# Kernel optimization log

Hardware: AMD Instinct MI355X
Metric: run time of the kernel (lower is better)

Reference implementation:

```python
import jax, jax.numpy as jnp
import numpy as np


def setup_inputs() -> dict:
    key = jax.random.key(0)
    k0, k1, k2, k3 = jax.random.split(key, 4)
    B, S, D, F, E = 2, 2048, 1024, 4096, 8
    scale = 0.02
    return {
        "x": jax.random.normal(k0, (B, S, D), jnp.float32),
        "gate_w": jax.random.normal(k1, (E, D), jnp.float32) * scale,
        "gate_b": jnp.zeros((E,), jnp.float32),
        "w1": jax.random.normal(k2, (E, D, F), jnp.float32) * scale,
        "b1": jnp.zeros((E, F), jnp.float32),
        "w2": jax.random.normal(k3, (E, F, D), jnp.float32) * scale,
        "b2": jnp.zeros((E, D), jnp.float32),
        "top_k": 2,
    }


def reference(x, gate_w, gate_b, w1, b1, w2, b2, top_k):
    B, S, D = x.shape
    E = gate_w.shape[0]
    xt = x.reshape(-1, D)                                   # [T, D]
    T = xt.shape[0]

    # Router: softmax over gate logits, then top-k and renormalize.
    gate_probs = jax.nn.softmax(xt @ gate_w.T + gate_b, axis=-1)   # [T, E]
    weights, selected = jax.lax.top_k(gate_probs, top_k)           # [T, k]
    weights = weights / jnp.sum(weights, axis=-1, keepdims=True)

    # Per-token combine weights over experts (zero where not selected),
    # equivalent to the per-expert gather/scatter loop in the original.
    combine = jnp.zeros((T, E), x.dtype).at[
        jnp.arange(T)[:, None], selected
    ].add(weights)                                                 # [T, E]

    # Expert MLPs (dense over experts, masked combine).
    h = jax.nn.silu(jnp.einsum("td,edf->etf", xt, w1) + b1[:, None, :])  # [E, T, F]
    expert_out = jnp.einsum("etf,efd->etd", h, w2) + b2[:, None, :]      # [E, T, D]
    out = jnp.einsum("etd,te->td", expert_out, combine)                  # [T, D]
    return out.reshape(B, S, D)
```

## Files before the change

kernel.cpp:

```cpp
#include <hip/hip_runtime.h>

#define T_TOK 4096
#define DIM   1024
#define FDIM  4096
#define NEXP  8

typedef __bf16 bf16x8 __attribute__((ext_vector_type(8)));
typedef __bf16 bf16x4 __attribute__((ext_vector_type(4)));
typedef float  f32x4  __attribute__((ext_vector_type(4)));

__device__ __forceinline__ void glds16(const void* g, void* l) {
    __builtin_amdgcn_global_load_lds(
        (const __attribute__((address_space(1))) void*)g,
        (__attribute__((address_space(3))) void*)l, 16, 0, 0);
}

__device__ __forceinline__ int xcd_swz(int phys, int total) {
    int q = total >> 3, r = total & 7;
    int x = phys & 7, i = phys >> 3;
    return (x < r ? x * (q + 1) : r * (q + 1) + (x - r) * q) + i;
}

__global__ __launch_bounds__(64)
void moe_router(const float* __restrict__ x,
                const float* __restrict__ gw,
                const float* __restrict__ gb,
                const int*   __restrict__ topk_p,
                int*   __restrict__ counts,
                int*   __restrict__ bucket,
                float* __restrict__ bweight,
                __bf16* __restrict__ xb) {
    const int t = blockIdx.x;
    const int lane = threadIdx.x;
    float part[NEXP];
#pragma unroll
    for (int e = 0; e < NEXP; ++e) part[e] = 0.f;
    const float* xrow = x + (size_t)t * DIM;
    __bf16* xbrow = xb + (size_t)t * DIM;
#pragma unroll
    for (int r = 0; r < 4; ++r) {
        int c = r * 256 + lane * 4;
        float4 v = *(const float4*)&xrow[c];
        bf16x4 o; o[0]=(__bf16)v.x; o[1]=(__bf16)v.y; o[2]=(__bf16)v.z; o[3]=(__bf16)v.w;
        *(bf16x4*)&xbrow[c] = o;
#pragma unroll
        for (int e = 0; e < NEXP; ++e) {
            float4 g = *(const float4*)&gw[e * DIM + c];
            part[e] += v.x*g.x + v.y*g.y + v.z*g.z + v.w*g.w;
        }
    }
#pragma unroll
    for (int off = 32; off > 0; off >>= 1) {
#pragma unroll
        for (int e = 0; e < NEXP; ++e) part[e] += __shfl_xor(part[e], off);
    }
    if (lane == 0) {
        int k = topk_p[0];
        if (k < 1) k = 1;
        if (k > NEXP) k = NEXP;
        float p[NEXP];
        float mx = -1e30f;
#pragma unroll
        for (int e = 0; e < NEXP; ++e) {
            p[e] = part[e] + gb[e];
            mx = fmaxf(mx, p[e]);
        }
#pragma unroll
        for (int e = 0; e < NEXP; ++e) p[e] = __expf(p[e] - mx);
        bool used[NEXP];
#pragma unroll
        for (int e = 0; e < NEXP; ++e) used[e] = false;
        int sel[NEXP]; float selp[NEXP]; float wsum = 0.f;
        for (int j = 0; j < k; ++j) {
            int best = 0; float bv = -1.f;
            for (int e = 0; e < NEXP; ++e)
                if (!used[e] && p[e] > bv) { bv = p[e]; best = e; }
            used[best] = true; sel[j] = best; selp[j] = bv; wsum += bv;
        }
        for (int j = 0; j < k; ++j) {
            int e = sel[j];
            int pos = atomicAdd(&counts[e], 1);
            bucket[e * T_TOK + pos]  = t;
            bweight[e * T_TOK + pos] = selp[j] / wsum;
        }
    }
}

__global__ __launch_bounds__(256)
void transpose_cvt(const float* __restrict__ in, __bf16* __restrict__ out,
                   int R, int C) {
    const size_t zo = (size_t)blockIdx.z * R * C;
    in += zo; out += zo;
    __shared__ float ts[64][65];
    const int c0 = blockIdx.x * 64, r0 = blockIdx.y * 64;
    const int t = threadIdx.x;
    const int rr = t >> 2, cc4 = (t & 3) * 16;
    const float* src = in + (size_t)(r0 + rr) * C + c0 + cc4;
#pragma unroll
    for (int i = 0; i < 4; ++i) {
        float4 v = *(const float4*)(src + i * 4);
        ts[rr][cc4 + i*4 + 0] = v.x; ts[rr][cc4 + i*4 + 1] = v.y;
        ts[rr][cc4 + i*4 + 2] = v.z; ts[rr][cc4 + i*4 + 3] = v.w;
    }
    __syncthreads();
    const int oc = rr, orc = cc4;
    bf16x8 o0, o1;
#pragma unroll
    for (int i = 0; i < 8; ++i) o0[i] = (__bf16)ts[orc + i][oc];
#pragma unroll
    for (int i = 0; i < 8; ++i) o1[i] = (__bf16)ts[orc + 8 + i][oc];
    __bf16* dst = out + (size_t)(c0 + oc) * R + r0 + orc;
    *(bf16x8*)dst = o0;
    *(bf16x8*)(dst + 8) = o1;
}

__global__ __launch_bounds__(64)
void build_work(const int* __restrict__ counts, int* __restrict__ hdr) {
    __shared__ int off1[NEXP + 1];
    const int lane = threadIdx.x;
    if (lane == 0) {
        int a = 0;
        for (int e = 0; e < NEXP; ++e) {
            off1[e] = a;
            a += (counts[e] + 255) >> 8;
        }
        off1[NEXP] = a;
        hdr[0] = a;
    }
    __syncthreads();
    for (int e = 0; e < NEXP; ++e) {
        int n1 = off1[e + 1] - off1[e];
        for (int j = lane; j < n1; j += 64) hdr[8 + off1[e] + j] = (e << 16) | j;
    }
}


__global__ __launch_bounds__(512, 2)
void moe_gemm1(const __bf16* __restrict__ xb,
               const __bf16* __restrict__ w1t,
               const float*  __restrict__ b1,
               const int*    __restrict__ counts,
               const int*    __restrict__ bucket,
               const int*    __restrict__ hdr,
               __bf16* __restrict__ H) {
    __shared__ __align__(16) char sb[3 * 32768];
    __shared__ int tok_s[256];
    const int tid = threadIdx.x;
    const int wave = tid >> 6, lane = tid & 63;
    const int wm = wave & 1, wn = wave >> 1;
    const int quad = lane >> 4, l15 = lane & 15;
    const int lrow = lane >> 2;
    const int rr  = tid >> 2;
    const int srh = ((tid & 3) ^ ((tid >> 3) & 3)) * 8;
    const int swz16 = (((lane >> 4) ^ ((lane >> 1) & 3)) << 4);
    const int aoff = (wm * 128 + l15) * 64 + swz16;
    const int boff = (wn * 64  + l15) * 64 + swz16;

    const int NT = DIM / 32;
    const int n1 = hdr[0];
    const int total = n1 * (FDIM / 256);
    for (int phys = blockIdx.x; phys < total; phys += gridDim.x) {
        const int u = xcd_swz(phys, total);
        const int entry = hdr[8 + (u % n1)];
        const int e = entry >> 16, tile = entry & 0xffff;
        const int nb = (u / n1) * 256;
        const int cnt = counts[e];
        for (int r = tid; r < 256; r += 512) {
            int rw = tile * 256 + r;
            if (rw >= cnt) rw = cnt - 1;
            tok_s[r] = bucket[e * T_TOK + rw];
        }
        __syncthreads();

        const __bf16* pa0 = xb + (size_t)tok_s[rr]       * DIM + srh;
        const __bf16* pa1 = xb + (size_t)tok_s[rr + 128] * DIM + srh;
        const __bf16* pb0 = w1t + ((size_t)e * FDIM + nb + rr) * DIM + srh;
        const __bf16* pb1 = pb0 + (size_t)128 * DIM;

        f32x4 acc[8][4];
#pragma unroll
        for (int i = 0; i < 8; ++i)
#pragma unroll
            for (int j = 0; j < 4; ++j) acc[i][j] = (f32x4){0.f,0.f,0.f,0.f};

#pragma unroll
        for (int p = 0; p < 2; ++p) {
            char* db = sb + p * 32768;
            const int ko = p * 32;
            glds16(pa0 + ko, db + wave * 1024);
            glds16(pa1 + ko, db + 8192 + wave * 1024);
            glds16(pb0 + ko, db + 16384 + wave * 1024);
            glds16(pb1 + ko, db + 24576 + wave * 1024);
        }

        int bc = 0, bn = 2;
#pragma unroll 1
        for (int t = 0; t < NT; ++t) {
            if (t + 2 < NT) {
                char* db = sb + bn * 32768;
                const int ko = (t + 2) * 32;
                glds16(pa0 + ko, db + wave * 1024);
                glds16(pa1 + ko, db + 8192 + wave * 1024);
                glds16(pb0 + ko, db + 16384 + wave * 1024);
                glds16(pb1 + ko, db + 24576 + wave * 1024);
                asm volatile("s_waitcnt vmcnt(8)" ::: "memory");
            } else if (t + 2 == NT) {
                asm volatile("s_waitcnt vmcnt(4)" ::: "memory");
            } else {
                asm volatile("s_waitcnt vmcnt(0)" ::: "memory");
            }
            __builtin_amdgcn_s_barrier();
            asm volatile("" ::: "memory");

            const char* Ab = sb + bc * 32768;
            const char* Bb = Ab + 16384;
            bf16x8 af[8], bfr[4];
#pragma unroll
            for (int i = 0; i < 8; ++i)
                af[i] = *(const bf16x8*)(Ab + aoff + i * 1024);
#pragma unroll
            for (int j = 0; j < 4; ++j)
                bfr[j] = *(const bf16x8*)(Bb + boff + j * 1024);
            __builtin_amdgcn_s_setprio(1);
#pragma unroll
            for (int i = 0; i < 8; ++i)
#pragma unroll
                for (int j = 0; j < 4; ++j)
                    acc[i][j] = __builtin_amdgcn_mfma_f32_16x16x32_bf16(
                        af[i], bfr[j], acc[i][j], 0, 0, 0);
            __builtin_amdgcn_s_setprio(0);

            asm volatile("" ::: "memory");
            __builtin_amdgcn_s_barrier();
            bc = (bc == 2) ? 0 : bc + 1;
            bn = (bn == 2) ? 0 : bn + 1;
        }

        __bf16* stg = (__bf16*)(sb + wave * 2304);
        const float* b1e = b1 + e * FDIM + nb + wn * 64;
#pragma unroll
        for (int i = 0; i < 8; ++i) {
#pragma unroll
            for (int j = 0; j < 4; ++j) {
                float bias = b1e[j * 16 + l15];
#pragma unroll
                for (int r = 0; r < 4; ++r) {
                    float v = acc[i][j][r] + bias;
                    float s = v / (1.f + __expf(-v));
                    stg[(quad*4 + r) * 72 + j*16 + l15] = (__bf16)s;
                }
            }
            int prow = tile * 256 + wm * 128 + i * 16 + lrow;
            if (prow < cnt) {
                bf16x8 v0 = *(const bf16x8*)&stg[lrow * 72 + (lane & 3) * 16];
                bf16x8 v1 = *(const bf16x8*)&stg[lrow * 72 + (lane & 3) * 16 + 8];
                __bf16* dst = H + (size_t)(e * T_TOK + prow) * FDIM
                              + nb + wn * 64 + (lane & 3) * 16;
                *(bf16x8*)dst = v0;
                *(bf16x8*)(dst + 8) = v1;
            }
        }
        __syncthreads();
    }
}

#define KSPLIT 2
#define KHALF  (FDIM / KSPLIT)

__global__ __launch_bounds__(512, 2)
void moe_gemm2(const __bf16* __restrict__ H,
               const __bf16* __restrict__ w2t,
               const float*  __restrict__ b2,
               const int*    __restrict__ counts,
               const int*    __restrict__ bucket,
               const float*  __restrict__ bweight,
               const int*    __restrict__ hdr,
               float* __restrict__ out) {
    __shared__ __align__(16) char sb[3 * 32768];
    __shared__ int   tok_s[256];
    __shared__ float w_s[256];
    const int tid = threadIdx.x;
    const int wave = tid >> 6, lane = tid & 63;
    const int wm = wave & 1, wn = wave >> 1;
    const int quad = lane >> 4, l15 = lane & 15;
    const int rr  = tid >> 2;
    const int srh = ((tid & 3) ^ ((tid >> 3) & 3)) * 8;
    const int swz16 = (((lane >> 4) ^ ((lane >> 1) & 3)) << 4);
    const int aoff = (wm * 128 + l15) * 64 + swz16;
    const int boff = (wn * 64  + l15) * 64 + swz16;

    const int NT = KHALF / 32;
    const int n1 = hdr[0];
    const int total = n1 * (DIM / 256) * KSPLIT;
    for (int phys = blockIdx.x; phys < total; phys += gridDim.x) {
        const int u = xcd_swz(phys, total);
        const int entry = hdr[8 + (u % n1)];
        const int e = entry >> 16, tile = entry & 0xffff;
        const int rest = u / n1;
        const int nb = (rest & 3) * 256;
        const int kc = rest >> 2;
        const int cnt = counts[e];
        for (int r = tid; r < 256; r += 512) {
            int rw = tile * 256 + r;
            int rc = rw < cnt ? rw : cnt - 1;
            tok_s[r] = bucket[e * T_TOK + rc];
            w_s[r]   = bweight[e * T_TOK + rc];
        }
        __syncthreads();

        const size_t kbase = (size_t)kc * KHALF;
        const __bf16* pa0 = H + (size_t)(e * T_TOK + tile * 256 + rr) * FDIM + kbase + srh;
        const __bf16* pa1 = pa0 + (size_t)128 * FDIM;
        const __bf16* pb0 = w2t + ((size_t)e * DIM + nb + rr) * FDIM + kbase + srh;
        const __bf16* pb1 = pb0 + (size_t)128 * FDIM;

        f32x4 acc[8][4];
#pragma unroll
        for (int i = 0; i < 8; ++i)
#pragma unroll
            for (int j = 0; j < 4; ++j) acc[i][j] = (f32x4){0.f,0.f,0.f,0.f};

#pragma unroll
        for (int p = 0; p < 2; ++p) {
            char* db = sb + p * 32768;
            const int ko = p * 32;
            glds16(pa0 + ko, db + wave * 1024);
            glds16(pa1 + ko, db + 8192 + wave * 1024);
            glds16(pb0 + ko, db + 16384 + wave * 1024);
            glds16(pb1 + ko, db + 24576 + wave * 1024);
        }

        int bc = 0, bn = 2;
#pragma unroll 1
        for (int t = 0; t < NT; ++t) {
            if (t + 2 < NT) {
                char* db = sb + bn * 32768;
                const int ko = (t + 2) * 32;
                glds16(pa0 + ko, db + wave * 1024);
                glds16(pa1 + ko, db + 8192 + wave * 1024);
                glds16(pb0 + ko, db + 16384 + wave * 1024);
                glds16(pb1 + ko, db + 24576 + wave * 1024);
                asm volatile("s_waitcnt vmcnt(8)" ::: "memory");
            } else if (t + 2 == NT) {
                asm volatile("s_waitcnt vmcnt(4)" ::: "memory");
            } else {
                asm volatile("s_waitcnt vmcnt(0)" ::: "memory");
            }
            __builtin_amdgcn_s_barrier();
            asm volatile("" ::: "memory");

            const char* Ab = sb + bc * 32768;
            const char* Bb = Ab + 16384;
            bf16x8 af[8], bfr[4];
#pragma unroll
            for (int i = 0; i < 8; ++i)
                af[i] = *(const bf16x8*)(Ab + aoff + i * 1024);
#pragma unroll
            for (int j = 0; j < 4; ++j)
                bfr[j] = *(const bf16x8*)(Bb + boff + j * 1024);
            __builtin_amdgcn_s_setprio(1);
#pragma unroll
            for (int i = 0; i < 8; ++i)
#pragma unroll
                for (int j = 0; j < 4; ++j)
                    acc[i][j] = __builtin_amdgcn_mfma_f32_16x16x32_bf16(
                        af[i], bfr[j], acc[i][j], 0, 0, 0);
            __builtin_amdgcn_s_setprio(0);

            asm volatile("" ::: "memory");
            __builtin_amdgcn_s_barrier();
            bc = (bc == 2) ? 0 : bc + 1;
            bn = (bn == 2) ? 0 : bn + 1;
        }

        float bias[4];
#pragma unroll
        for (int j = 0; j < 4; ++j)
            bias[j] = (kc == 0) ? b2[e * DIM + nb + wn * 64 + j * 16 + l15] : 0.f;
#pragma unroll
        for (int i = 0; i < 8; ++i)
#pragma unroll
            for (int j = 0; j < 4; ++j)
#pragma unroll
                for (int r = 0; r < 4; ++r) {
                    int m = wm * 128 + i * 16 + quad * 4 + r;
                    int prow = tile * 256 + m;
                    if (prow < cnt) {
                        int dc = nb + wn * 64 + j * 16 + l15;
                        float v = acc[i][j][r] + bias[j];
                        atomicAdd(&out[(size_t)tok_s[m] * DIM + dc], w_s[m] * v);
                    }
                }
        __syncthreads();
    }
}

extern "C" void kernel_launch(void* const* d_in, const int* in_sizes, int n_in,
                              void* d_out, int out_size, void* d_ws, size_t ws_size,
                              hipStream_t stream) {
    const float* x  = (const float*)d_in[0];
    const float* gw = (const float*)d_in[1];
    const float* gb = (const float*)d_in[2];
    const float* w1 = (const float*)d_in[3];
    const float* b1 = (const float*)d_in[4];
    const float* w2 = (const float*)d_in[5];
    const float* b2 = (const float*)d_in[6];
    const int* topk = (const int*)d_in[7];
    float* out = (float*)d_out;

    char* ws = (char*)d_ws;
    size_t off = 0;
    int* counts = (int*)(ws + off);    off += 256;
    int* bucket = (int*)(ws + off);    off += (size_t)NEXP * T_TOK * 4;
    float* bw   = (float*)(ws + off);  off += (size_t)NEXP * T_TOK * 4;
    int* hdr    = (int*)(ws + off);    off += 4096;
    off = (off + 255) & ~(size_t)255;
    __bf16* xb  = (__bf16*)(ws + off); off += (size_t)T_TOK * DIM * 2;
    __bf16* w1t = (__bf16*)(ws + off); off += (size_t)NEXP * DIM * FDIM * 2;
    __bf16* w2t = (__bf16*)(ws + off); off += (size_t)NEXP * FDIM * DIM * 2;
    __bf16* H   = (__bf16*)(ws + off);

    hipMemsetAsync(counts, 0, 256, stream);
    hipMemsetAsync(out, 0, (size_t)out_size * 4, stream);

    moe_router<<<T_TOK, 64, 0, stream>>>(x, gw, gb, topk, counts, bucket, bw, xb);
    transpose_cvt<<<dim3(FDIM/64, DIM/64, NEXP), 256, 0, stream>>>(w1, w1t, DIM, FDIM);
    transpose_cvt<<<dim3(DIM/64, FDIM/64, NEXP), 256, 0, stream>>>(w2, w2t, FDIM, DIM);
    build_work<<<1, 64, 0, stream>>>(counts, hdr);

    moe_gemm1<<<256, 512, 0, stream>>>(xb, w1t, b1, counts, bucket, hdr, H);
    moe_gemm2<<<256, 512, 0, stream>>>(H, w2t, b2, counts, bucket, bw, hdr, out);
}
```

Baseline: 833.0 us.

## Deepen the LDS prefetch pipeline to four stages and hand-issue the ds_read_b128 loads

Both expert GEMM kernels grow the shared-memory ring from 3 to 4 tiles. The global-to-LDS prefetch now runs three K-steps ahead, with adjusted vmcnt waits, so more global-load latency can hide behind MFMA work. Fragment loads become inline-asm ds_read_b128 instructions with immediate offsets, followed by one lgkmcnt(0) wait and a sched_barrier, which removes per-load address arithmetic. The cost is more LDS per block (128KB) and a fixed schedule that stops the compiler from overlapping LDS reads with MFMAs.

```diff
diff --git a/kernel.cpp b/kernel.cpp
--- a/kernel.cpp
+++ b/kernel.cpp
@@ -8,12 +8,16 @@
 typedef __bf16 bf16x8 __attribute__((ext_vector_type(8)));
 typedef __bf16 bf16x4 __attribute__((ext_vector_type(4)));
 typedef float  f32x4  __attribute__((ext_vector_type(4)));
+typedef const __attribute__((address_space(3))) char* lds3;
 
 __device__ __forceinline__ void glds16(const void* g, void* l) {
     __builtin_amdgcn_global_load_lds(
         (const __attribute__((address_space(1))) void*)g,
         (__attribute__((address_space(3))) void*)l, 16, 0, 0);
 }
+
+#define DSR(dst, a, imm) \
+    asm volatile("ds_read_b128 %0, %1 offset:" #imm : "=v"(dst) : "v"(a) : "memory")
 
 __device__ __forceinline__ int xcd_swz(int phys, int total) {
     int q = total >> 3, r = total & 7;
@@ -143,7 +147,7 @@
                const int*    __restrict__ bucket,
                const int*    __restrict__ hdr,
                __bf16* __restrict__ H) {
-    __shared__ __align__(16) char sb[3 * 32768];
+    __shared__ __align__(16) char sb[4 * 32768];
     __shared__ int tok_s[256];
     const int tid = threadIdx.x;
     const int wave = tid >> 6, lane = tid & 63;
@@ -154,7 +158,8 @@
     const int srh = ((tid & 3) ^ ((tid >> 3) & 3)) * 8;
     const int swz16 = (((lane >> 4) ^ ((lane >> 1) & 3)) << 4);
     const int aoff = (wm * 128 + l15) * 64 + swz16;
-    const int boff = (wn * 64  + l15) * 64 + swz16;
+    const int boff = 16384 + (wn * 64 + l15) * 64 + swz16;
+    lds3 s3 = (lds3)sb;
 
     const int NT = DIM / 32;
     const int n1 = hdr[0];
@@ -184,7 +189,7 @@
             for (int j = 0; j < 4; ++j) acc[i][j] = (f32x4){0.f,0.f,0.f,0.f};
 
 #pragma unroll
-        for (int p = 0; p < 2; ++p) {
+        for (int p = 0; p < 3; ++p) {
             char* db = sb + p * 32768;
             const int ko = p * 32;
             glds16(pa0 + ko, db + wave * 1024);
@@ -193,16 +198,18 @@
             glds16(pb1 + ko, db + 24576 + wave * 1024);
         }
 
-        int bc = 0, bn = 2;
 #pragma unroll 1
         for (int t = 0; t < NT; ++t) {
-            if (t + 2 < NT) {
-                char* db = sb + bn * 32768;
-                const int ko = (t + 2) * 32;
+            const int bc = t & 3;
+            if (t + 3 < NT) {
+                char* db = sb + ((t + 3) & 3) * 32768;
+                const int ko = (t + 3) * 32;
                 glds16(pa0 + ko, db + wave * 1024);
                 glds16(pa1 + ko, db + 8192 + wave * 1024);
                 glds16(pb0 + ko, db + 16384 + wave * 1024);
                 glds16(pb1 + ko, db + 24576 + wave * 1024);
+                asm volatile("s_waitcnt vmcnt(12)" ::: "memory");
+            } else if (t + 3 == NT) {
                 asm volatile("s_waitcnt vmcnt(8)" ::: "memory");
             } else if (t + 2 == NT) {
                 asm volatile("s_waitcnt vmcnt(4)" ::: "memory");
@@ -210,17 +217,19 @@
                 asm volatile("s_waitcnt vmcnt(0)" ::: "memory");
             }
             __builtin_amdgcn_s_barrier();
-            asm volatile("" ::: "memory");
-
-            const char* Ab = sb + bc * 32768;
-            const char* Bb = Ab + 16384;
+
+            lds3 a3 = s3 + bc * 32768 + aoff;
+            lds3 b3 = s3 + bc * 32768 + boff;
             bf16x8 af[8], bfr[4];
-#pragma unroll
-            for (int i = 0; i < 8; ++i)
-                af[i] = *(const bf16x8*)(Ab + aoff + i * 1024);
-#pragma unroll
-            for (int j = 0; j < 4; ++j)
-                bfr[j] = *(const bf16x8*)(Bb + boff + j * 1024);
+            DSR(af[0], a3, 0);    DSR(af[1], a3, 1024);
+            DSR(af[2], a3, 2048); DSR(af[3], a3, 3072);
+            DSR(af[4], a3, 4096); DSR(af[5], a3, 5120);
+            DSR(af[6], a3, 6144); DSR(af[7], a3, 7168);
+            DSR(bfr[0], b3, 0);    DSR(bfr[1], b3, 1024);
+            DSR(bfr[2], b3, 2048); DSR(bfr[3], b3, 3072);
+            asm volatile("s_waitcnt lgkmcnt(0)" ::: "memory");
+            __builtin_amdgcn_sched_barrier(0);
+
             __builtin_amdgcn_s_setprio(1);
 #pragma unroll
             for (int i = 0; i < 8; ++i)
@@ -229,11 +238,7 @@
                     acc[i][j] = __builtin_amdgcn_mfma_f32_16x16x32_bf16(
                         af[i], bfr[j], acc[i][j], 0, 0, 0);
             __builtin_amdgcn_s_setprio(0);
-
-            asm volatile("" ::: "memory");
             __builtin_amdgcn_s_barrier();
-            bc = (bc == 2) ? 0 : bc + 1;
-            bn = (bn == 2) ? 0 : bn + 1;
         }
 
         __bf16* stg = (__bf16*)(sb + wave * 2304);
@@ -276,7 +281,7 @@
                const float*  __restrict__ bweight,
                const int*    __restrict__ hdr,
                float* __restrict__ out) {
-    __shared__ __align__(16) char sb[3 * 32768];
+    __shared__ __align__(16) char sb[4 * 32768];
     __shared__ int   tok_s[256];
     __shared__ float w_s[256];
     const int tid = threadIdx.x;
@@ -287,7 +292,8 @@
     const int srh = ((tid & 3) ^ ((tid >> 3) & 3)) * 8;
     const int swz16 = (((lane >> 4) ^ ((lane >> 1) & 3)) << 4);
     const int aoff = (wm * 128 + l15) * 64 + swz16;
-    const int boff = (wn * 64  + l15) * 64 + swz16;
+    const int boff = 16384 + (wn * 64 + l15) * 64 + swz16;
+    lds3 s3 = (lds3)sb;
 
     const int NT = KHALF / 32;
     const int n1 = hdr[0];
@@ -321,7 +327,7 @@
             for (int j = 0; j < 4; ++j) acc[i][j] = (f32x4){0.f,0.f,0.f,0.f};
 
 #pragma unroll
-        for (int p = 0; p < 2; ++p) {
+        for (int p = 0; p < 3; ++p) {
             char* db = sb + p * 32768;
             const int ko = p * 32;
             glds16(pa0 + ko, db + wave * 1024);
@@ -330,16 +336,18 @@
             glds16(pb1 + ko, db + 24576 + wave * 1024);
         }
 
-        int bc = 0, bn = 2;
 #pragma unroll 1
         for (int t = 0; t < NT; ++t) {
-            if (t + 2 < NT) {
-                char* db = sb + bn * 32768;
-                const int ko = (t + 2) * 32;
+            const int bc = t & 3;
+            if (t + 3 < NT) {
+                char* db = sb + ((t + 3) & 3) * 32768;
+                const int ko = (t + 3) * 32;
                 glds16(pa0 + ko, db + wave * 1024);
                 glds16(pa1 + ko, db + 8192 + wave * 1024);
                 glds16(pb0 + ko, db + 16384 + wave * 1024);
                 glds16(pb1 + ko, db + 24576 + wave * 1024);
+                asm volatile("s_waitcnt vmcnt(12)" ::: "memory");
+            } else if (t + 3 == NT) {
                 asm volatile("s_waitcnt vmcnt(8)" ::: "memory");
             } else if (t + 2 == NT) {
                 asm volatile("s_waitcnt vmcnt(4)" ::: "memory");
@@ -347,17 +355,19 @@
                 asm volatile("s_waitcnt vmcnt(0)" ::: "memory");
             }
             __builtin_amdgcn_s_barrier();
-            asm volatile("" ::: "memory");
-
-            const char* Ab = sb + bc * 32768;
-            const char* Bb = Ab + 16384;
+
+            lds3 a3 = s3 + bc * 32768 + aoff;
+            lds3 b3 = s3 + bc * 32768 + boff;
             bf16x8 af[8], bfr[4];
-#pragma unroll
-            for (int i = 0; i < 8; ++i)
-                af[i] = *(const bf16x8*)(Ab + aoff + i * 1024);
-#pragma unroll
-            for (int j = 0; j < 4; ++j)
-                bfr[j] = *(const bf16x8*)(Bb + boff + j * 1024);
+            DSR(af[0], a3, 0);    DSR(af[1], a3, 1024);
+            DSR(af[2], a3, 2048); DSR(af[3], a3, 3072);
+            DSR(af[4], a3, 4096); DSR(af[5], a3, 5120);
+            DSR(af[6], a3, 6144); DSR(af[7], a3, 7168);
+            DSR(bfr[0], b3, 0);    DSR(bfr[1], b3, 1024);
+            DSR(bfr[2], b3, 2048); DSR(bfr[3], b3, 3072);
+            asm volatile("s_waitcnt lgkmcnt(0)" ::: "memory");
+            __builtin_amdgcn_sched_barrier(0);
+
             __builtin_amdgcn_s_setprio(1);
 #pragma unroll
             for (int i = 0; i < 8; ++i)
@@ -366,11 +376,7 @@
                     acc[i][j] = __builtin_amdgcn_mfma_f32_16x16x32_bf16(
                         af[i], bfr[j], acc[i][j], 0, 0, 0);
             __builtin_amdgcn_s_setprio(0);
-
-            asm volatile("" ::: "memory");
             __builtin_amdgcn_s_barrier();
-            bc = (bc == 2) ? 0 : bc + 1;
-            bn = (bn == 2) ? 0 : bn + 1;
         }
 
         float bias[4];
```

After: 771.9 us. -7.3%, faster.
